# Optimization experiments

Measured on AMD Instinct MI355X. Metric: run time of the kernel, lower is better.

The kernel has to match this reference:

```python
import jax, jax.numpy as jnp
from jax import lax
import numpy as np

EPS = 1e-5
NH = 16  # attention heads (c // 16 with c = 256)


def _qconv(x, mod, phase, padding=0, groups=1):
    """Quaternion conv: real weight = modulus * cos(phase), applied per quaternion component.
    x: (B, C, Q, H, W) -> (B, O, Q, H, W)"""
    w = mod * jnp.cos(phase)
    B, C, Qd, H, W = x.shape
    xr = jnp.transpose(x, (0, 2, 1, 3, 4)).reshape(B * Qd, C, H, W)
    y = lax.conv_general_dilated(xr, w, (1, 1), [(padding, padding)] * 2,
                                 dimension_numbers=('NCHW', 'OIHW', 'NCHW'),
                                 feature_group_count=groups)
    O, Ho, Wo = y.shape[1], y.shape[2], y.shape[3]
    return jnp.transpose(y.reshape(B, Qd, O, Ho, Wo), (0, 2, 1, 3, 4))


def _bn(x):
    # IQBN/VQBN: per-channel normalization over (batch, quaternion, spatial), no affine
    m = x.mean(axis=(0, 2, 3, 4), keepdims=True)
    v = x.var(axis=(0, 2, 3, 4), keepdims=True)
    return (x - m) * lax.rsqrt(v + EPS)


def _attn(x, qkv_m, qkv_p, aproj_m, aproj_p, pe_m, pe_p):
    # QAttention: per-component multi-head self-attention over spatial tokens
    B, C, Qd, H, W = x.shape
    kd = C // NH
    qkv = _qconv(x, qkv_m, qkv_p)  # (B, 3C, Q, H, W)
    q, k, v = jnp.split(qkv, 3, axis=1)
    q = q.reshape(B, NH, kd, Qd, H * W)
    k = k.reshape(B, NH, kd, Qd, H * W)
    v = v.reshape(B, NH, kd, Qd, H * W)
    scores = jnp.einsum('bhcqn,bhcqm->bhqnm', q, k) * (kd ** -0.5)
    a = jax.nn.softmax(scores, axis=-1)
    out = jnp.einsum('bhqnm,bhdqm->bhdqn', a, v).reshape(B, C, Qd, H, W)
    # proj + depthwise positional conv on the input
    return _qconv(out, aproj_m, aproj_p) + _qconv(x, pe_m, pe_p, padding=1, groups=C)


def _psa(x, qkv_m, qkv_p, aproj_m, aproj_p, pe_m, pe_p, ffn1_m, ffn1_p, ffn2_m, ffn2_p):
    a = _attn(x, qkv_m, qkv_p, aproj_m, aproj_p, pe_m, pe_p) + x  # attn shortcut
    h = jax.nn.relu(_bn(_qconv(a, ffn1_m, ffn1_p)))
    f = _bn(_qconv(h, ffn2_m, ffn2_p))
    return f + a  # ffn shortcut


def _msab(x, guide, ec_m, ec_p, gl_w, gl_b, mproj_m, mproj_p):
    # MaxSigmoidAttnBlock (nh=1): global sigmoid gate per (batch, quaternion component)
    B, C, Qd, H, W = x.shape
    e = jax.nn.relu(_bn(_qconv(x, ec_m, ec_p)))  # (B, ec, Q, H, W)
    g = guide @ gl_w.T + gl_b                     # (B, ec)
    ec = g.shape[-1]
    a = jnp.einsum('bcqhw,bc->bq', e, g) / jnp.sqrt(jnp.asarray(ec * H * W, jnp.float32))
    a = jax.nn.sigmoid(a)  # scale param = 1.0 (scale=False)
    e = e * a[:, None, :, None, None]
    return jax.nn.relu(_bn(_qconv(e, mproj_m, mproj_p, padding=1)))


def _forward(x, guide, cv1_m, cv1_p, qkv_m, qkv_p, aproj_m, aproj_p, pe_m, pe_p,
             ffn1_m, ffn1_p, ffn2_m, ffn2_p, ec_m, ec_p, gl_w, gl_b,
             mproj_m, mproj_p, cv2_m, cv2_p):
    y = jax.nn.relu(_bn(_qconv(x, cv1_m, cv1_p)))       # (B, 2c, Q, H, W)
    a, b = jnp.split(y, 2, axis=1)                       # each (B, c, Q, H, W)
    p = _psa(b, qkv_m, qkv_p, aproj_m, aproj_p, pe_m, pe_p,
             ffn1_m, ffn1_p, ffn2_m, ffn2_p)
    m = _msab(p, guide, ec_m, ec_p, gl_w, gl_b, mproj_m, mproj_p)
    cat = jnp.concatenate([a, b, p, m], axis=1)          # (B, 4c, Q, H, W)
    return jax.nn.relu(_bn(_qconv(cat, cv2_m, cv2_p)))   # (B, c2, Q, H, W)


def setup_inputs():
    B, C1, Qd, H, W = 2, 512, 4, 24, 24
    c = 256; ecd = 128; gc = 512; C2 = 512
    ks = jax.random.split(jax.random.key(0), 24)
    def rp(k, shape, s=0.02):
        return s * jax.random.normal(k, shape, dtype=jnp.float32)
    return {
        'x': jax.random.normal(ks[0], (B, C1, Qd, H, W), dtype=jnp.float32),
        'guide': jax.random.normal(ks[1], (B, gc), dtype=jnp.float32),
        'cv1_m': rp(ks[2], (2 * c, C1, 1, 1)),
        'cv1_p': rp(ks[3], (2 * c, C1, 1, 1), 0.1),
        'qkv_m': rp(ks[4], (3 * c, c, 1, 1)),
        'qkv_p': rp(ks[5], (3 * c, c, 1, 1), 0.1),
        'aproj_m': rp(ks[6], (c, c, 1, 1)),
        'aproj_p': rp(ks[7], (c, c, 1, 1), 0.1),
        'pe_m': rp(ks[8], (c, 1, 3, 3)),
        'pe_p': rp(ks[9], (c, 1, 3, 3), 0.1),
        'ffn1_m': rp(ks[10], (2 * c, c, 1, 1)),
        'ffn1_p': rp(ks[11], (2 * c, c, 1, 1), 0.1),
        'ffn2_m': rp(ks[12], (c, 2 * c, 1, 1)),
        'ffn2_p': rp(ks[13], (c, 2 * c, 1, 1), 0.1),
        'ec_m': rp(ks[14], (ecd, c, 1, 1)),
        'ec_p': rp(ks[15], (ecd, c, 1, 1), 0.1),
        'gl_w': rp(ks[16], (ecd, gc), 0.05),
        'gl_b': jnp.zeros((ecd,), dtype=jnp.float32),
        'mproj_m': rp(ks[17], (c, ecd, 3, 3)),
        'mproj_p': rp(ks[18], (c, ecd, 3, 3), 0.1),
        'cv2_m': rp(ks[19], (C2, 4 * c, 1, 1)),
        'cv2_p': rp(ks[20], (C2, 4 * c, 1, 1), 0.1),
    }


def reference(x, guide, cv1_m, cv1_p, qkv_m, qkv_p, aproj_m, aproj_p, pe_m, pe_p,
              ffn1_m, ffn1_p, ffn2_m, ffn2_p, ec_m, ec_p, gl_w, gl_b,
              mproj_m, mproj_p, cv2_m, cv2_p):
    return _forward(x, guide, cv1_m, cv1_p, qkv_m, qkv_p, aproj_m, aproj_p, pe_m, pe_p,
                    ffn1_m, ffn1_p, ffn2_m, ffn2_p, ec_m, ec_p, gl_w, gl_b,
                    mproj_m, mproj_p, cv2_m, cv2_p)
```

## Files before the change

### kernel.cpp

```cpp
#include <hip/hip_runtime.h>
#include <math.h>

typedef __bf16 bf16x8 __attribute__((ext_vector_type(8)));
typedef float f32x4 __attribute__((ext_vector_type(4)));
typedef unsigned short u16;
typedef unsigned int u32;

__device__ __forceinline__ u16 f2bf(float f) {
  u32 u = __float_as_uint(f);
  u32 r = u + 0x7FFF + ((u >> 16) & 1);
  return (u16)(r >> 16);
}
__device__ __forceinline__ float bf2f(u16 h) { return __uint_as_float(((u32)h) << 16); }

static constexpr size_t OB_WBF = 0;
static constexpr size_t OB_WPE = 3276800;
static constexpr size_t OB_ST  = 3286016;
static constexpr size_t OB_GV  = 3310592;
static constexpr size_t OB_GACC= 3311616;
static constexpr size_t OB_CAT = 3311872;
static constexpr size_t OB_YA  = OB_CAT + 9437184;
static constexpr size_t OB_U1  = OB_YA + 9437184;
static constexpr size_t OB_U2  = OB_U1 + 4718592;
static constexpr size_t OB_U3  = OB_U2 + 14155776;
static constexpr size_t OB_AOB = OB_U3 + 4718592;
static constexpr size_t OB_A1B = OB_AOB + 2359296;
static constexpr size_t WS_TOTAL = OB_A1B + 2359296;

struct HeadP {
  const float* m[8]; const float* p[8]; u16* wout;
  const float* pem; const float* pep; float* peout;
  const float* x; u16* xb;
  const float* guide; const float* glw; const float* glb; float* gv;
  int cum[9]; int nwp;
};
__global__ __launch_bounds__(256) void k_head(HeadP P) {
  int bid = blockIdx.x;
  if (bid < P.nwp) {
    int i = bid * 256 + threadIdx.x;
    if (i < 2304) {
      int tap = i >> 8, c = i & 255;
      P.peout[i] = P.pem[c * 9 + tap] * cosf(P.pep[c * 9 + tap]);
    }
    if (i >= P.cum[8]) return;
    int s = 0;
    while (s < 7 && i >= P.cum[s + 1]) s++;
    int j = i - P.cum[s];
    int src = j;
    if (s == 6) {
      int o = j / 1152, r = j % 1152, kk = r >> 7, cc = r & 127;
      src = (o * 128 + cc) * 9 + kk;
    }
    P.wout[i] = f2bf(P.m[s][src] * cosf(P.p[s][src]));
    return;
  }
  bid -= P.nwp;
  if (bid < 2304) {
    int mt = bid % 18; bid /= 18;
    int ct = bid % 16; bid /= 16;
    int q = bid & 3, b = bid >> 2;
    __shared__ float tile[32][33];
    int tj = threadIdx.x & 31, ti = threadIdx.x >> 5;
    const float* xp = P.x + (((size_t)(b * 512 + ct * 32) * 4 + q) * 576) + mt * 32;
#pragma unroll
    for (int ii = 0; ii < 4; ii++)
      tile[ti + ii * 8][tj] = xp[(size_t)(ti + ii * 8) * 4 * 576 + tj];
    __syncthreads();
    u16* yp = P.xb + ((size_t)b * 2304 + q * 576 + mt * 32) * 512 + ct * 32;
#pragma unroll
    for (int mm = 0; mm < 4; mm++)
      yp[(size_t)(mm * 8 + ti) * 512 + tj] = f2bf(tile[tj][mm * 8 + ti]);
    return;
  }
  bid -= 2304;
  int wv = threadIdx.x >> 6, lane = threadIdx.x & 63;
  int be = bid * 4 + wv;
  int b = be >> 7, e = be & 127;
  const float* gr = P.guide + b * 512;
  const float* wr = P.glw + e * 512;
  float s = 0.f;
  for (int c = lane; c < 512; c += 64) s = fmaf(gr[c], wr[c], s);
#pragma unroll
  for (int off = 32; off > 0; off >>= 1) s += __shfl_down(s, off, 64);
  if (lane == 0) P.gv[be] = s + P.glb[e];
}

struct GemmP {
  const u16* W; const u16* X; u16* Yb; float* St;
  const u16* CAT; const float* W9;
  const u16* EF; const float* GA;
  long long xOff[8];
  int lda, O, K, M, G;
};

template <int BM, int NWO, int WO, int WM, int MODE>
__global__ __launch_bounds__(256) void k_gemm(GemmP P) {
  constexpr int FO = WO / 16, FM = WM / 16;
  constexpr int OBLK = NWO * WO;
  constexpr int ABYTES = OBLK * 128, BBYTES = BM * 128;
  __shared__ __align__(16) char lds[2 * ABYTES + 2 * BBYTES];
  const int mt = P.M / BM;
  const int ot = P.O / OBLK;
  int bid = blockIdx.x;
  const int g = bid / (mt * ot);
  const int rr = bid % (mt * ot);
  const int ob = (rr / mt) * OBLK;
  const int mb = (rr % mt) * BM;
  const int t = threadIdx.x, lane = t & 63, wave = t >> 6;
  const int wo = (wave % NWO) * WO, wm = (wave / NWO) * WM;
  const u16* Wp = P.W + (size_t)ob * P.K;
  const u16* Xp = (MODE == 2) ? nullptr : (P.X + P.xOff[g] + (size_t)mb * P.lda);

  float gt = 0.f;
  int bq2304 = 0;
  if constexpr (MODE == 2) {
    bq2304 = (g >> 2) * 2304 + (g & 3) * 576;
    float a = P.GA[g] / sqrtf(73728.0f);
    gt = 1.f / (1.f + __expf(-a));
  }

  f32x4 acc[FO][FM] = {};
  float vreg[2][8];

  auto stageA = [&](int tb, int k0) {
#pragma unroll
    for (int i = 0; i < OBLK * 8 / 256; i++) {
      int s = (i * 4 + wave) * 64 + lane;
      int row = s >> 3;
      int kg = (s & 7) ^ (row & 7);
      const u16* src = Wp + (size_t)row * P.K + k0 + kg * 8;
      __builtin_amdgcn_global_load_lds(
          (const __attribute__((address_space(1))) u32*)src,
          (__attribute__((address_space(3))) u32*)(lds + tb * ABYTES + (size_t)(i * 4 + wave) * 1024),
          16, 0, 0);
    }
  };
  auto stageB = [&](int tb, int k0) {
#pragma unroll
    for (int i = 0; i < BM * 8 / 256; i++) {
      int s = (i * 4 + wave) * 64 + lane;
      int row = s >> 3;
      int kg = (s & 7) ^ (row & 7);
      const u16* src = Xp + (size_t)row * P.lda + k0 + kg * 8;
      __builtin_amdgcn_global_load_lds(
          (const __attribute__((address_space(1))) u32*)src,
          (__attribute__((address_space(3))) u32*)(lds + 2 * ABYTES + tb * BBYTES +
                                                   (size_t)(i * 4 + wave) * 1024),
          16, 0, 0);
    }
  };
  auto loadEF = [&](int k0) {
#pragma unroll
    for (int i = 0; i < 2; i++) {
      int s = t + i * 256;
      int row = s >> 3, kg = s & 7;
      int k = k0 + kg * 8;
      int kk = k >> 7, cc = k & 127;
      int n = mb + row;
      int h = n / 24 + kk / 3 - 1, w = n % 24 + kk % 3 - 1;
      if (h >= 0 && h < 24 && w >= 0 && w < 24) {
        const u16* ep = P.EF + ((size_t)(bq2304 + h * 24 + w)) * 128 + cc;
        ushort4 v0 = *(const ushort4*)ep;
        ushort4 v1 = *(const ushort4*)(ep + 4);
        vreg[i][0] = bf2f(v0.x); vreg[i][1] = bf2f(v0.y);
        vreg[i][2] = bf2f(v0.z); vreg[i][3] = bf2f(v0.w);
        vreg[i][4] = bf2f(v1.x); vreg[i][5] = bf2f(v1.y);
        vreg[i][6] = bf2f(v1.z); vreg[i][7] = bf2f(v1.w);
      } else {
#pragma unroll
        for (int j = 0; j < 8; j++) vreg[i][j] = 0.f;
      }
    }
  };
  auto writeB = [&](int tb) {
#pragma unroll
    for (int i = 0; i < 2; i++) {
      int s = t + i * 256;
      int row = s >> 3, kg = s & 7;
      u16 pk[8];
#pragma unroll
      for (int j = 0; j < 8; j++) pk[j] = f2bf(vreg[i][j] * gt);
      *(uint4*)&lds[2 * ABYTES + tb * BBYTES + (((row << 3) + (kg ^ (row & 7))) << 4)] =
          *(uint4*)pk;
    }
  };

  const int nt = P.K >> 6;
  stageA(0, 0);
  if constexpr (MODE != 2) {
    stageB(0, 0);
  } else {
    loadEF(0);
    writeB(0);
  }
  __syncthreads();

  for (int tt = 0; tt < nt; tt++) {
    const int cur = tt & 1, nxt = cur ^ 1;
    const bool more = (tt + 1) < nt;
    if (more) {
      stageA(nxt, (tt + 1) << 6);
      if constexpr (MODE != 2) stageB(nxt, (tt + 1) << 6);
      else loadEF((tt + 1) << 6);
    }
    const char* bA = lds + cur * ABYTES;
    const char* bB = lds + 2 * ABYTES + cur * BBYTES;
#pragma unroll
    for (int kk = 0; kk < 2; kk++) {
      int kgl = kk * 4 + (lane >> 4);
      bf16x8 af[FO], bfm[FM];
#pragma unroll
      for (int fo = 0; fo < FO; fo++) {
        int row = wo + fo * 16 + (lane & 15);
        af[fo] = *(bf16x8*)&bA[((row << 3) + (kgl ^ (row & 7))) << 4];
      }
#pragma unroll
      for (int fm = 0; fm < FM; fm++) {
        int row = wm + fm * 16 + (lane & 15);
        bfm[fm] = *(bf16x8*)&bB[((row << 3) + (kgl ^ (row & 7))) << 4];
      }
#pragma unroll
      for (int fo = 0; fo < FO; fo++)
#pragma unroll
        for (int fm = 0; fm < FM; fm++)
          acc[fo][fm] = __builtin_amdgcn_mfma_f32_16x16x32_bf16(af[fo], bfm[fm], acc[fo][fm], 0, 0, 0);
    }
    if (more) {
      if constexpr (MODE == 2) writeB(nxt);
      __syncthreads();
    }
  }

  size_t ybase = (size_t)g * P.M * P.O;
#pragma unroll
  for (int fo = 0; fo < FO; fo++) {
    int ow = ob + wo + fo * 16 + ((lane >> 4) << 2);
#pragma unroll
    for (int fm = 0; fm < FM; fm++) {
      int m = mb + wm + fm * 16 + (lane & 15);
      f32x4 v = acc[fo][fm];
      if constexpr (MODE == 1) {
        size_t tokc = ((size_t)g * 2304 + m) * 1024 + 256 + ow;
        ushort4 cv = *(const ushort4*)&P.CAT[tokc];
        v[0] += bf2f(cv.x); v[1] += bf2f(cv.y); v[2] += bf2f(cv.z); v[3] += bf2f(cv.w);
        int q_ = m / 576, hw_ = m % 576, h_ = hw_ / 24, w_ = hw_ % 24;
        size_t rowb = ((size_t)g * 2304 + q_ * 576) * 1024 + 256 + ow;
#pragma unroll
        for (int tp = 0; tp < 9; tp++) {
          int hh = h_ + tp / 3 - 1, ww = w_ + tp % 3 - 1;
          if (hh < 0 || hh > 23 || ww < 0 || ww > 23) continue;
          ushort4 tv = *(const ushort4*)&P.CAT[rowb + (size_t)(hh * 24 + ww) * 1024];
          f32x4 wt = *(const f32x4*)&P.W9[tp * 256 + ow];
          v[0] = fmaf(wt[0], bf2f(tv.x), v[0]);
          v[1] = fmaf(wt[1], bf2f(tv.y), v[1]);
          v[2] = fmaf(wt[2], bf2f(tv.z), v[2]);
          v[3] = fmaf(wt[3], bf2f(tv.w), v[3]);
        }
        acc[fo][fm] = v;
      }
      size_t off = ybase + (size_t)m * P.O + ow;
      ushort4 r;
      r.x = f2bf(v[0]); r.y = f2bf(v[1]); r.z = f2bf(v[2]); r.w = f2bf(v[3]);
      *(ushort4*)&P.Yb[off] = r;
    }
  }

  if (P.St) {
#pragma unroll
    for (int fo = 0; fo < FO; fo++) {
      float sv[4], qv[4];
#pragma unroll
      for (int j = 0; j < 4; j++) { sv[j] = 0.f; qv[j] = 0.f; }
#pragma unroll
      for (int fm = 0; fm < FM; fm++)
#pragma unroll
        for (int j = 0; j < 4; j++) {
          float a = acc[fo][fm][j];
          sv[j] += a;
          qv[j] = fmaf(a, a, qv[j]);
        }
#pragma unroll
      for (int j = 0; j < 4; j++) {
#pragma unroll
        for (int mk = 1; mk < 16; mk <<= 1) {
          sv[j] += __shfl_xor(sv[j], mk, 64);
          qv[j] += __shfl_xor(qv[j], mk, 64);
        }
      }
      if ((lane & 15) == 0) {
        int o = ob + wo + fo * 16 + ((lane >> 4) << 2);
#pragma unroll
        for (int j = 0; j < 4; j++) {
          atomicAdd(&P.St[2 * (o + j)], sv[j]);
          atomicAdd(&P.St[2 * (o + j) + 1], qv[j]);
        }
      }
    }
  }
}

struct NormP {
  const u16* X; const float* st; const u16* AddB;
  u16* Yb; u16* Yfb; const float* gv; float* gacc;
  long long ybOff[8];
  int ldyb, O, G, M, relu;
  float n;
};
__global__ __launch_bounds__(256) void k_norm(NormP P) {
  int O4 = P.O >> 2;
  long long idx = (long long)blockIdx.x * 256 + threadIdx.x;
  if (idx >= (long long)P.G * P.M * O4) return;
  int c4 = (int)(idx % O4);
  long long gm = idx / O4;
  int m = (int)(gm % P.M);
  int g = (int)(gm / P.M);
  size_t off = (size_t)gm * P.O + c4 * 4;
  ushort4 xv = *(const ushort4*)&P.X[off];
  f32x4 v = {bf2f(xv.x), bf2f(xv.y), bf2f(xv.z), bf2f(xv.w)};
  float inv_n = 1.0f / P.n;
#pragma unroll
  for (int j = 0; j < 4; j++) {
    int c = c4 * 4 + j;
    float mean = P.st[2 * c] * inv_n;
    float var = P.st[2 * c + 1] * inv_n - mean * mean;
    v[j] = (v[j] - mean) * rsqrtf(var + 1e-5f);
  }
  if (P.AddB) {
    ushort4 av = *(const ushort4*)(P.AddB + off);
    v[0] += bf2f(av.x); v[1] += bf2f(av.y); v[2] += bf2f(av.z); v[3] += bf2f(av.w);
  }
  if (P.relu) {
#pragma unroll
    for (int j = 0; j < 4; j++) v[j] = fmaxf(v[j], 0.f);
  }
  ushort4 r;
  r.x = f2bf(v[0]); r.y = f2bf(v[1]); r.z = f2bf(v[2]); r.w = f2bf(v[3]);
  if (P.Yb) *(ushort4*)(P.Yb + P.ybOff[g] + (size_t)m * P.ldyb + c4 * 4) = r;
  if (P.Yfb) *(ushort4*)(P.Yfb + off) = r;
  if (P.gacc) {
    float gs = 0.f;
#pragma unroll
    for (int j = 0; j < 4; j++) gs = fmaf(v[j], P.gv[g * 128 + c4 * 4 + j], gs);
#pragma unroll
    for (int mk = 1; mk < 64; mk <<= 1) gs += __shfl_xor(gs, mk, 64);
    __shared__ float t1[4];
    int lane = threadIdx.x & 63, wv = threadIdx.x >> 6;
    if (lane == 0) t1[wv] = gs;
    __syncthreads();
    if (threadIdx.x == 0)
      atomicAdd(&P.gacc[g * 4 + m / 576], t1[0] + t1[1] + t1[2] + t1[3]);
  }
}

__global__ __launch_bounds__(256) void k_normT(const u16* X, const float* st, float* out) {
  int bid = blockIdx.x;
  int ot = bid & 15;
  int mt = (bid >> 4) % 72;
  int b = bid / 1152;
  int mb = mt * 32, ob = ot * 32;
  __shared__ float tile[32][33];
  int c = threadIdx.x & 31, r = threadIdx.x >> 5;
#pragma unroll
  for (int i = 0; i < 4; i++) {
    int row = r + i * 8;
    tile[row][c] = bf2f(X[((size_t)b * 2304 + mb + row) * 512 + ob + c]);
  }
  __syncthreads();
  float inv_n = 1.0f / 4608.0f;
#pragma unroll
  for (int i = 0; i < 4; i++) {
    int o = ob + r + i * 8;
    float mean = st[2 * o] * inv_n;
    float var = st[2 * o + 1] * inv_n - mean * mean;
    float rs = rsqrtf(var + 1e-5f);
    float v = fmaxf((tile[c][r + i * 8] - mean) * rs, 0.f);
    out[((size_t)(b * 512 + o)) * 2304 + mb + c] = v;
  }
}

__global__ __launch_bounds__(256) void k_attn(const u16* qkv, u16* ao) {
  int bid = blockIdx.x;
  int tq = bid % 3; int u = bid / 3;
  int qd = u & 3; u >>= 2;
  int head = u & 15, b = u >> 4;
  int t = threadIdx.x, lane = t & 63, wv = t >> 6;
  int g = lane >> 4, q = lane & 15;
  size_t tok0 = (size_t)b * 2304 + qd * 576;
  const u16* QKV = qkv + tok0 * 768;

  __shared__ __align__(16) char shm[50176];
  u16* Kl = (u16*)(shm);
  u16* VT = (u16*)(shm + 27648);
  u16* Pl = (u16*)(shm + 46080 + wv * 1024);

  for (int i = t; i < 1152; i += 256) {
    int m = i >> 1, half = i & 1;
    const u16* src = QKV + (size_t)m * 768 + 256 + head * 16 + half * 8;
    u16 tmp[8];
    *(uint4*)tmp = *(const uint4*)src;
    ushort4 lo, hi;
    lo.x = f2bf(bf2f(tmp[0]) * 0.25f); lo.y = f2bf(bf2f(tmp[1]) * 0.25f);
    lo.z = f2bf(bf2f(tmp[2]) * 0.25f); lo.w = f2bf(bf2f(tmp[3]) * 0.25f);
    hi.x = f2bf(bf2f(tmp[4]) * 0.25f); hi.y = f2bf(bf2f(tmp[5]) * 0.25f);
    hi.z = f2bf(bf2f(tmp[6]) * 0.25f); hi.w = f2bf(bf2f(tmp[7]) * 0.25f);
    u16* dst = Kl + m * 24 + half * 8;
    *(ushort4*)dst = lo;
    *(ushort4*)(dst + 4) = hi;
  }
  for (int mm = t; mm < 576; mm += 256) {
    const u16* src = QKV + (size_t)mm * 768 + 512 + head * 16;
    u16 tmp[16];
    *(uint4*)tmp = *(const uint4*)src;
    *(uint4*)(tmp + 8) = *(const uint4*)(src + 8);
    u16* dst = VT + (mm >> 3) * 128 + (mm & 7);
#pragma unroll
    for (int d = 0; d < 16; d++) dst[d * 8] = tmp[d];
  }
  __syncthreads();

#pragma unroll 1
  for (int i = 0; i < 3; i++) {
    int tl = wv * 3 + i;
    int qbase = tq * 192 + tl * 16;
    bf16x8 qf = {};
    if (g < 2)
      qf = *(const bf16x8*)(QKV + (size_t)(qbase + q) * 768 + head * 16 + g * 8);

    f32x4 acc_o = {};
    float ssum = 0.f;

    for (int ch = 0; ch < 18; ch++) {
      int m0 = ch * 32;
      f32x4 s[2];
#pragma unroll
      for (int h = 0; h < 2; h++) {
        bf16x8 kf = {};
        if (g < 2)
          kf = *(const bf16x8*)(Kl + (size_t)(m0 + h * 16 + q) * 24 + g * 8);
        f32x4 z = {};
        s[h] = __builtin_amdgcn_mfma_f32_16x16x32_bf16(kf, qf, z, 0, 0, 0);
      }
#pragma unroll
      for (int h = 0; h < 2; h++) {
        float p0 = __expf(s[h][0]);
        float p1 = __expf(s[h][1]);
        float p2 = __expf(s[h][2]);
        float p3 = __expf(s[h][3]);
        ssum += (p0 + p1) + (p2 + p3);
        ushort4 w;
        w.x = f2bf(p0); w.y = f2bf(p1); w.z = f2bf(p2); w.w = f2bf(p3);
        *(ushort4*)(Pl + ((h * 2 + (g >> 1)) * 16 + q) * 8 + (g & 1) * 4) = w;
      }
      bf16x8 va = *(const bf16x8*)(VT + ((m0 >> 3) + g) * 128 + q * 8);
      bf16x8 pa = *(const bf16x8*)(Pl + (g * 16 + q) * 8);
      acc_o = __builtin_amdgcn_mfma_f32_16x16x32_bf16(va, pa, acc_o, 0, 0, 0);
    }

    ssum += __shfl_xor(ssum, 16, 64);
    ssum += __shfl_xor(ssum, 32, 64);
    float inv = 1.f / ssum;
    u16* op = ao + (tok0 + qbase + q) * 256 + head * 16 + g * 4;
    ushort4 r;
    r.x = f2bf(acc_o[0] * inv);
    r.y = f2bf(acc_o[1] * inv);
    r.z = f2bf(acc_o[2] * inv);
    r.w = f2bf(acc_o[3] * inv);
    *(ushort4*)op = r;
  }
}

extern "C" void kernel_launch(void* const* d_in, const int* in_sizes, int n_in,
                              void* d_out, int out_size, void* d_ws, size_t ws_size,
                              hipStream_t stream) {
  if (ws_size < WS_TOTAL) return;
  char* ws = (char*)d_ws;
  u16* WB = (u16*)(ws + OB_WBF);
  float* WPE = (float*)(ws + OB_WPE);
  float* STB = (float*)(ws + OB_ST);
  float* GV = (float*)(ws + OB_GV);
  float* GACC = (float*)(ws + OB_GACC);
  u16* CATB = (u16*)(ws + OB_CAT);
  u16* YAB = (u16*)(ws + OB_YA);
  u16* XBF = (u16*)(ws + OB_U1);
  u16* QKVB = (u16*)(ws + OB_U2);
  u16* EFB = (u16*)(ws + OB_U2 + 10616832);
  u16* HB = (u16*)(ws + OB_U3);
  u16* AOB = (u16*)(ws + OB_AOB);
  u16* A1B = (u16*)(ws + OB_A1B);
  float* out = (float*)d_out;

  hipMemsetAsync(ws + OB_ST, 0, OB_CAT - OB_ST, stream);

  {
    HeadP p;
    const int mi[8] = {2, 4, 6, 10, 12, 14, 18, 20};
    const int sz[8] = {262144, 196608, 65536, 131072, 131072, 32768, 294912, 524288};
    int c = 0;
    for (int i = 0; i < 8; i++) {
      p.m[i] = (const float*)d_in[mi[i]];
      p.p[i] = (const float*)d_in[mi[i] + 1];
      p.cum[i] = c;
      c += sz[i];
    }
    p.cum[8] = c;
    p.wout = WB;
    p.pem = (const float*)d_in[8];
    p.pep = (const float*)d_in[9];
    p.peout = WPE;
    p.x = (const float*)d_in[0];
    p.xb = XBF;
    p.guide = (const float*)d_in[1];
    p.glw = (const float*)d_in[16];
    p.glb = (const float*)d_in[17];
    p.gv = GV;
    p.nwp = (c + 255) / 256;
    int grid = p.nwp + 2304 + 64;
    k_head<<<grid, 256, 0, stream>>>(p);
  }

  auto gemm = [&](int mode, size_t wOff, int O, int K, int M, int G,
                  const u16* X, long long xs, long long xadd, int lda,
                  u16* Yb, int si) {
    GemmP p;
    p.W = WB + wOff; p.X = X; p.Yb = Yb;
    p.St = (si >= 0) ? (STB + si * 1024) : nullptr;
    p.CAT = CATB; p.W9 = WPE; p.EF = EFB; p.GA = GACC;
    p.lda = lda; p.O = O; p.K = K; p.M = M; p.G = G;
    for (int g = 0; g < 8; g++) p.xOff[g] = (long long)(g < G ? g : 0) * xs + xadd;
    int grid = G * (O / 128) * (M / 64);
    if (mode == 0)
      k_gemm<64, 4, 32, 64, 0><<<grid, 256, 0, stream>>>(p);
    else if (mode == 1)
      k_gemm<64, 4, 32, 64, 1><<<grid, 256, 0, stream>>>(p);
    else
      k_gemm<64, 4, 32, 64, 2><<<grid, 256, 0, stream>>>(p);
  };
  auto norm = [&](const u16* X, int si, int O, int G, int M, const u16* AddB,
                  u16* Yb, int ldyb, const long long* ybOff, u16* Yfb, int relu,
                  const float* gv, float* gacc) {
    NormP p;
    p.X = X; p.st = STB + si * 1024; p.AddB = AddB; p.Yb = Yb; p.Yfb = Yfb;
    p.gv = gv; p.gacc = gacc;
    p.ldyb = ldyb; p.O = O; p.G = G; p.M = M; p.relu = relu;
    p.n = (float)(G * M);
    for (int g = 0; g < 8; g++) p.ybOff[g] = ybOff ? ybOff[(g < G) ? g : 0] : 0;
    long long total = (long long)G * M * (O / 4);
    k_norm<<<(int)((total + 255) / 256), 256, 0, stream>>>(p);
  };

  gemm(0, 0, 512, 512, 2304, 2, XBF, 2304LL * 512, 0, 512, YAB, 0);
  { long long yo[2] = {0, 2304LL * 1024};
    norm(YAB, 0, 512, 2, 2304, nullptr, CATB, 1024, yo, nullptr, 1, nullptr, nullptr); }

  gemm(0, 262144, 768, 256, 2304, 2, CATB, 2304LL * 1024, 256, 1024, QKVB, -1);
  k_attn<<<384, 256, 0, stream>>>(QKVB, AOB);
  gemm(1, 458752, 256, 256, 2304, 2, AOB, 2304LL * 256, 0, 256, A1B, -1);

  gemm(0, 524288, 512, 256, 2304, 2, A1B, 2304LL * 256, 0, 256, YAB, 1);
  { long long yo[2] = {0, 2304LL * 512};
    norm(YAB, 1, 512, 2, 2304, nullptr, HB, 512, yo, nullptr, 1, nullptr, nullptr); }

  gemm(0, 655360, 256, 512, 2304, 2, HB, 2304LL * 512, 0, 512, YAB, 2);
  { long long yo[2] = {512, 2304LL * 1024 + 512};
    norm(YAB, 2, 256, 2, 2304, A1B, CATB, 1024, yo, nullptr, 0, nullptr, nullptr); }

  gemm(0, 786432, 128, 256, 2304, 2, CATB, 2304LL * 1024, 512, 1024, YAB, 3);
  norm(YAB, 3, 128, 2, 2304, nullptr, nullptr, 0, nullptr, EFB, 1, GV, GACC);

  gemm(2, 819200, 256, 1152, 576, 8, nullptr, 0, 0, 0, YAB, 4);
  { long long yo[8];
    for (int g = 0; g < 8; g++)
      yo[g] = (long long)(g >> 2) * 2304 * 1024 + (long long)(g & 3) * 576 * 1024 + 768;
    norm(YAB, 4, 256, 8, 576, nullptr, CATB, 1024, yo, nullptr, 1, nullptr, nullptr); }

  gemm(0, 1114112, 512, 1024, 2304, 2, CATB, 2304LL * 1024, 0, 1024, YAB, 5);
  k_normT<<<2304, 256, 0, stream>>>(YAB, STB + 5 * 1024, out);
}
```

Before: 259.3 us.

## Fuse batch-norm epilogues into GEMMs using an atomic grid-wide barrier

```diff
diff --git a/kernel.cpp b/kernel.cpp
--- a/kernel.cpp
+++ b/kernel.cpp
@@ -18,6 +18,7 @@
 static constexpr size_t OB_ST  = 3286016;
 static constexpr size_t OB_GV  = 3310592;
 static constexpr size_t OB_GACC= 3311616;
+static constexpr size_t OB_CTR = 3311744;
 static constexpr size_t OB_CAT = 3311872;
 static constexpr size_t OB_YA  = OB_CAT + 9437184;
 static constexpr size_t OB_U1  = OB_YA + 9437184;
@@ -89,11 +90,12 @@
   const u16* W; const u16* X; u16* Yb; float* St;
   const u16* CAT; const float* W9;
   const u16* EF; const float* GA;
-  long long xOff[8];
-  int lda, O, K, M, G;
+  const u16* AddB; const float* gv; float* gacc; float* outF; u32* ctr;
+  long long xOff[8]; long long yOff2[8];
+  int lda, O, K, M, G, ldyb, relu, nblk;
 };
 
-template <int BM, int NWO, int WO, int WM, int MODE>
+template <int BM, int NWO, int WO, int WM, int MODE, int NEPI>
 __global__ __launch_bounds__(256) void k_gemm(GemmP P) {
   constexpr int FO = WO / 16, FM = WM / 16;
   constexpr int OBLK = NWO * WO;
@@ -231,41 +233,42 @@
     }
   }
 
+  const int lane15 = lane & 15, laneh = (lane >> 4) << 2;
   size_t ybase = (size_t)g * P.M * P.O;
-#pragma unroll
-  for (int fo = 0; fo < FO; fo++) {
-    int ow = ob + wo + fo * 16 + ((lane >> 4) << 2);
-#pragma unroll
-    for (int fm = 0; fm < FM; fm++) {
-      int m = mb + wm + fm * 16 + (lane & 15);
-      f32x4 v = acc[fo][fm];
-      if constexpr (MODE == 1) {
-        size_t tokc = ((size_t)g * 2304 + m) * 1024 + 256 + ow;
-        ushort4 cv = *(const ushort4*)&P.CAT[tokc];
-        v[0] += bf2f(cv.x); v[1] += bf2f(cv.y); v[2] += bf2f(cv.z); v[3] += bf2f(cv.w);
-        int q_ = m / 576, hw_ = m % 576, h_ = hw_ / 24, w_ = hw_ % 24;
-        size_t rowb = ((size_t)g * 2304 + q_ * 576) * 1024 + 256 + ow;
-#pragma unroll
-        for (int tp = 0; tp < 9; tp++) {
-          int hh = h_ + tp / 3 - 1, ww = w_ + tp % 3 - 1;
-          if (hh < 0 || hh > 23 || ww < 0 || ww > 23) continue;
-          ushort4 tv = *(const ushort4*)&P.CAT[rowb + (size_t)(hh * 24 + ww) * 1024];
-          f32x4 wt = *(const f32x4*)&P.W9[tp * 256 + ow];
-          v[0] = fmaf(wt[0], bf2f(tv.x), v[0]);
-          v[1] = fmaf(wt[1], bf2f(tv.y), v[1]);
-          v[2] = fmaf(wt[2], bf2f(tv.z), v[2]);
-          v[3] = fmaf(wt[3], bf2f(tv.w), v[3]);
+
+  if constexpr (NEPI == 0) {
+#pragma unroll
+    for (int fo = 0; fo < FO; fo++) {
+      int ow = ob + wo + fo * 16 + laneh;
+#pragma unroll
+      for (int fm = 0; fm < FM; fm++) {
+        int m = mb + wm + fm * 16 + lane15;
+        f32x4 v = acc[fo][fm];
+        if constexpr (MODE == 1) {
+          size_t tokc = ((size_t)g * 2304 + m) * 1024 + 256 + ow;
+          ushort4 cv = *(const ushort4*)&P.CAT[tokc];
+          v[0] += bf2f(cv.x); v[1] += bf2f(cv.y); v[2] += bf2f(cv.z); v[3] += bf2f(cv.w);
+          int q_ = m / 576, hw_ = m % 576, h_ = hw_ / 24, w_ = hw_ % 24;
+          size_t rowb = ((size_t)g * 2304 + q_ * 576) * 1024 + 256 + ow;
+#pragma unroll
+          for (int tp = 0; tp < 9; tp++) {
+            int hh = h_ + tp / 3 - 1, ww = w_ + tp % 3 - 1;
+            if (hh < 0 || hh > 23 || ww < 0 || ww > 23) continue;
+            ushort4 tv = *(const ushort4*)&P.CAT[rowb + (size_t)(hh * 24 + ww) * 1024];
+            f32x4 wt = *(const f32x4*)&P.W9[tp * 256 + ow];
+            v[0] = fmaf(wt[0], bf2f(tv.x), v[0]);
+            v[1] = fmaf(wt[1], bf2f(tv.y), v[1]);
+            v[2] = fmaf(wt[2], bf2f(tv.z), v[2]);
+            v[3] = fmaf(wt[3], bf2f(tv.w), v[3]);
+          }
         }
-        acc[fo][fm] = v;
-      }
-      size_t off = ybase + (size_t)m * P.O + ow;
-      ushort4 r;
-      r.x = f2bf(v[0]); r.y = f2bf(v[1]); r.z = f2bf(v[2]); r.w = f2bf(v[3]);
-      *(ushort4*)&P.Yb[off] = r;
-    }
-  }
-
-  if (P.St) {
+        size_t off = ybase + (size_t)m * P.O + ow;
+        ushort4 r;
+        r.x = f2bf(v[0]); r.y = f2bf(v[1]); r.z = f2bf(v[2]); r.w = f2bf(v[3]);
+        *(ushort4*)&P.Yb[off] = r;
+      }
+    }
+  } else {
 #pragma unroll
     for (int fo = 0; fo < FO; fo++) {
       float sv[4], qv[4];
@@ -287,8 +290,8 @@
           qv[j] += __shfl_xor(qv[j], mk, 64);
         }
       }
-      if ((lane & 15) == 0) {
-        int o = ob + wo + fo * 16 + ((lane >> 4) << 2);
+      if (lane15 == 0) {
+        int o = ob + wo + fo * 16 + laneh;
 #pragma unroll
         for (int j = 0; j < 4; j++) {
           atomicAdd(&P.St[2 * (o + j)], sv[j]);
@@ -296,85 +299,77 @@
         }
       }
     }
-  }
-}
-
-struct NormP {
-  const u16* X; const float* st; const u16* AddB;
-  u16* Yb; u16* Yfb; const float* gv; float* gacc;
-  long long ybOff[8];
-  int ldyb, O, G, M, relu;
-  float n;
-};
-__global__ __launch_bounds__(256) void k_norm(NormP P) {
-  int O4 = P.O >> 2;
-  long long idx = (long long)blockIdx.x * 256 + threadIdx.x;
-  if (idx >= (long long)P.G * P.M * O4) return;
-  int c4 = (int)(idx % O4);
-  long long gm = idx / O4;
-  int m = (int)(gm % P.M);
-  int g = (int)(gm / P.M);
-  size_t off = (size_t)gm * P.O + c4 * 4;
-  ushort4 xv = *(const ushort4*)&P.X[off];
-  f32x4 v = {bf2f(xv.x), bf2f(xv.y), bf2f(xv.z), bf2f(xv.w)};
-  float inv_n = 1.0f / P.n;
-#pragma unroll
-  for (int j = 0; j < 4; j++) {
-    int c = c4 * 4 + j;
-    float mean = P.st[2 * c] * inv_n;
-    float var = P.st[2 * c + 1] * inv_n - mean * mean;
-    v[j] = (v[j] - mean) * rsqrtf(var + 1e-5f);
-  }
-  if (P.AddB) {
-    ushort4 av = *(const ushort4*)(P.AddB + off);
-    v[0] += bf2f(av.x); v[1] += bf2f(av.y); v[2] += bf2f(av.z); v[3] += bf2f(av.w);
-  }
-  if (P.relu) {
-#pragma unroll
-    for (int j = 0; j < 4; j++) v[j] = fmaxf(v[j], 0.f);
-  }
-  ushort4 r;
-  r.x = f2bf(v[0]); r.y = f2bf(v[1]); r.z = f2bf(v[2]); r.w = f2bf(v[3]);
-  if (P.Yb) *(ushort4*)(P.Yb + P.ybOff[g] + (size_t)m * P.ldyb + c4 * 4) = r;
-  if (P.Yfb) *(ushort4*)(P.Yfb + off) = r;
-  if (P.gacc) {
+    __threadfence();
+    __syncthreads();
+    if (t == 0) {
+      atomicAdd(P.ctr, 1u);
+      while (atomicAdd(P.ctr, 0u) < (u32)P.nblk) __builtin_amdgcn_s_sleep(32);
+    }
+    __syncthreads();
+    __threadfence();
+
+    const float inv_n = 1.0f / 4608.0f;
+    float mn[FO][4], rs[FO][4];
+#pragma unroll
+    for (int fo = 0; fo < FO; fo++) {
+      int o = ob + wo + fo * 16 + laneh;
+#pragma unroll
+      for (int j = 0; j < 4; j++) {
+        float mean = P.St[2 * (o + j)] * inv_n;
+        float var = P.St[2 * (o + j) + 1] * inv_n - mean * mean;
+        mn[fo][j] = mean;
+        rs[fo][j] = rsqrtf(var + 1e-5f);
+      }
+    }
     float gs = 0.f;
 #pragma unroll
-    for (int j = 0; j < 4; j++) gs = fmaf(v[j], P.gv[g * 128 + c4 * 4 + j], gs);
-#pragma unroll
-    for (int mk = 1; mk < 64; mk <<= 1) gs += __shfl_xor(gs, mk, 64);
-    __shared__ float t1[4];
-    int lane = threadIdx.x & 63, wv = threadIdx.x >> 6;
-    if (lane == 0) t1[wv] = gs;
-    __syncthreads();
-    if (threadIdx.x == 0)
-      atomicAdd(&P.gacc[g * 4 + m / 576], t1[0] + t1[1] + t1[2] + t1[3]);
-  }
-}
-
-__global__ __launch_bounds__(256) void k_normT(const u16* X, const float* st, float* out) {
-  int bid = blockIdx.x;
-  int ot = bid & 15;
-  int mt = (bid >> 4) % 72;
-  int b = bid / 1152;
-  int mb = mt * 32, ob = ot * 32;
-  __shared__ float tile[32][33];
-  int c = threadIdx.x & 31, r = threadIdx.x >> 5;
-#pragma unroll
-  for (int i = 0; i < 4; i++) {
-    int row = r + i * 8;
-    tile[row][c] = bf2f(X[((size_t)b * 2304 + mb + row) * 512 + ob + c]);
-  }
-  __syncthreads();
-  float inv_n = 1.0f / 4608.0f;
-#pragma unroll
-  for (int i = 0; i < 4; i++) {
-    int o = ob + r + i * 8;
-    float mean = st[2 * o] * inv_n;
-    float var = st[2 * o + 1] * inv_n - mean * mean;
-    float rs = rsqrtf(var + 1e-5f);
-    float v = fmaxf((tile[c][r + i * 8] - mean) * rs, 0.f);
-    out[((size_t)(b * 512 + o)) * 2304 + mb + c] = v;
+    for (int fo = 0; fo < FO; fo++) {
+      int ow = ob + wo + fo * 16 + laneh;
+#pragma unroll
+      for (int fm = 0; fm < FM; fm++) {
+        int m = mb + wm + fm * 16 + lane15;
+        f32x4 v = acc[fo][fm];
+#pragma unroll
+        for (int j = 0; j < 4; j++) v[j] = (v[j] - mn[fo][j]) * rs[fo][j];
+        if constexpr (NEPI == 1) {
+          if (P.AddB) {
+            ushort4 av = *(const ushort4*)(P.AddB + ybase + (size_t)m * P.O + ow);
+            v[0] += bf2f(av.x); v[1] += bf2f(av.y); v[2] += bf2f(av.z); v[3] += bf2f(av.w);
+          }
+          if (P.relu) {
+#pragma unroll
+            for (int j = 0; j < 4; j++) v[j] = fmaxf(v[j], 0.f);
+          }
+          ushort4 r;
+          r.x = f2bf(v[0]); r.y = f2bf(v[1]); r.z = f2bf(v[2]); r.w = f2bf(v[3]);
+          *(ushort4*)(P.Yb + P.yOff2[g] + (size_t)m * P.ldyb + ow) = r;
+        } else if constexpr (NEPI == 2) {
+#pragma unroll
+          for (int j = 0; j < 4; j++) v[j] = fmaxf(v[j], 0.f);
+          ushort4 r;
+          r.x = f2bf(v[0]); r.y = f2bf(v[1]); r.z = f2bf(v[2]); r.w = f2bf(v[3]);
+          *(ushort4*)(P.Yb + ybase + (size_t)m * 128 + ow) = r;
+#pragma unroll
+          for (int j = 0; j < 4; j++) gs = fmaf(v[j], P.gv[g * 128 + ow + j], gs);
+        } else {
+#pragma unroll
+          for (int j = 0; j < 4; j++) {
+            float x = fmaxf(v[j], 0.f);
+            P.outF[(size_t)(g * 512 + ow + j) * 2304 + m] = x;
+          }
+        }
+      }
+    }
+    if constexpr (NEPI == 2) {
+#pragma unroll
+      for (int mk = 1; mk < 64; mk <<= 1) gs += __shfl_xor(gs, mk, 64);
+      float* red = (float*)lds;
+      __syncthreads();
+      if (lane == 0) red[wave] = gs;
+      __syncthreads();
+      if (t == 0)
+        atomicAdd(&P.gacc[g * 4 + mb / 576], red[0] + red[1] + red[2] + red[3]);
+    }
   }
 }
 
@@ -479,8 +474,8 @@
   float* STB = (float*)(ws + OB_ST);
   float* GV = (float*)(ws + OB_GV);
   float* GACC = (float*)(ws + OB_GACC);
+  u32* CTR = (u32*)(ws + OB_CTR);
   u16* CATB = (u16*)(ws + OB_CAT);
-  u16* YAB = (u16*)(ws + OB_YA);
   u16* XBF = (u16*)(ws + OB_U1);
   u16* QKVB = (u16*)(ws + OB_U2);
   u16* EFB = (u16*)(ws + OB_U2 + 10616832);
@@ -518,61 +513,57 @@
     k_head<<<grid, 256, 0, stream>>>(p);
   }
 
-  auto gemm = [&](int mode, size_t wOff, int O, int K, int M, int G,
+  auto gemm = [&](int mode, int nepi, size_t wOff, int O, int K, int M, int G,
                   const u16* X, long long xs, long long xadd, int lda,
-                  u16* Yb, int si) {
+                  u16* Yb, int si, const long long* yo2, int ldyb, int relu,
+                  const u16* AddB) {
     GemmP p;
     p.W = WB + wOff; p.X = X; p.Yb = Yb;
     p.St = (si >= 0) ? (STB + si * 1024) : nullptr;
+    p.ctr = (si >= 0) ? (CTR + si) : nullptr;
     p.CAT = CATB; p.W9 = WPE; p.EF = EFB; p.GA = GACC;
+    p.AddB = AddB; p.gv = GV; p.gacc = GACC; p.outF = out;
     p.lda = lda; p.O = O; p.K = K; p.M = M; p.G = G;
-    for (int g = 0; g < 8; g++) p.xOff[g] = (long long)(g < G ? g : 0) * xs + xadd;
+    p.ldyb = ldyb; p.relu = relu;
+    for (int g = 0; g < 8; g++) {
+      p.xOff[g] = (long long)(g < G ? g : 0) * xs + xadd;
+      p.yOff2[g] = yo2 ? yo2[(g < G) ? g : 0] : 0;
+    }
     int grid = G * (O / 128) * (M / 64);
-    if (mode == 0)
-      k_gemm<64, 4, 32, 64, 0><<<grid, 256, 0, stream>>>(p);
-    else if (mode == 1)
-      k_gemm<64, 4, 32, 64, 1><<<grid, 256, 0, stream>>>(p);
+    p.nblk = grid;
+    if (mode == 0 && nepi == 0)
+      k_gemm<64, 4, 32, 64, 0, 0><<<grid, 256, 0, stream>>>(p);
+    else if (mode == 1 && nepi == 0)
+      k_gemm<64, 4, 32, 64, 1, 0><<<grid, 256, 0, stream>>>(p);
+    else if (mode == 0 && nepi == 1)
+      k_gemm<64, 4, 32, 64, 0, 1><<<grid, 256, 0, stream>>>(p);
+    else if (mode == 2 && nepi == 1)
+      k_gemm<64, 4, 32, 64, 2, 1><<<grid, 256, 0, stream>>>(p);
+    else if (mode == 0 && nepi == 2)
+      k_gemm<64, 4, 32, 64, 0, 2><<<grid, 256, 0, stream>>>(p);
     else
-      k_gemm<64, 4, 32, 64, 2><<<grid, 256, 0, stream>>>(p);
+      k_gemm<64, 4, 32, 64, 0, 3><<<grid, 256, 0, stream>>>(p);
   };
-  auto norm = [&](const u16* X, int si, int O, int G, int M, const u16* AddB,
-                  u16* Yb, int ldyb, const long long* ybOff, u16* Yfb, int relu,
-                  const float* gv, float* gacc) {
-    NormP p;
-    p.X = X; p.st = STB + si * 1024; p.AddB = AddB; p.Yb = Yb; p.Yfb = Yfb;
-    p.gv = gv; p.gacc = gacc;
-    p.ldyb = ldyb; p.O = O; p.G = G; p.M = M; p.relu = relu;
-    p.n = (float)(G * M);
-    for (int g = 0; g < 8; g++) p.ybOff[g] = ybOff ? ybOff[(g < G) ? g : 0] : 0;
-    long long total = (long long)G * M * (O / 4);
-    k_norm<<<(int)((total + 255) / 256), 256, 0, stream>>>(p);
-  };
-
-  gemm(0, 0, 512, 512, 2304, 2, XBF, 2304LL * 512, 0, 512, YAB, 0);
+
   { long long yo[2] = {0, 2304LL * 1024};
-    norm(YAB, 0, 512, 2, 2304, nullptr, CATB, 1024, yo, nullptr, 1, nullptr, nullptr); }
-
-  gemm(0, 262144, 768, 256, 2304, 2, CATB, 2304LL * 1024, 256, 1024, QKVB, -1);
+    gemm(0, 1, 0, 512, 512, 2304, 2, XBF, 2304LL * 512, 0, 512, CATB, 0, yo, 1024, 1, nullptr); }
+
+  gemm(0, 0, 262144, 768, 256, 2304, 2, CATB, 2304LL * 1024, 256, 1024, QKVB, -1, nullptr, 0, 0, nullptr);
   k_attn<<<384, 256, 0, stream>>>(QKVB, AOB);
-  gemm(1, 458752, 256, 256, 2304, 2, AOB, 2304LL * 256, 0, 256, A1B, -1);
-
-  gemm(0, 524288, 512, 256, 2304, 2, A1B, 2304LL * 256, 0, 256, YAB, 1);
+  gemm(1, 0, 458752, 256, 256, 2304, 2, AOB, 2304LL * 256, 0, 256, A1B, -1, nullptr, 0, 0, nullptr);
+
   { long long yo[2] = {0, 2304LL * 512};
-    norm(YAB, 1, 512, 2, 2304, nullptr, HB, 512, yo, nullptr, 1, nullptr, nullptr); }
-
-  gemm(0, 655360, 256, 512, 2304, 2, HB, 2304LL * 512, 0, 512, YAB, 2);
+    gemm(0, 1, 524288, 512, 256, 2304, 2, A1B, 2304LL * 256, 0, 256, HB, 1, yo, 512, 1, nullptr); }
+
   { long long yo[2] = {512, 2304LL * 1024 + 512};
-    norm(YAB, 2, 256, 2, 2304, A1B, CATB, 1024, yo, nullptr, 0, nullptr, nullptr); }
-
-  gemm(0, 786432, 128, 256, 2304, 2, CATB, 2304LL * 1024, 512, 1024, YAB, 3);
-  norm(YAB, 3, 128, 2, 2304, nullptr, nullptr, 0, nullptr, EFB, 1, GV, GACC);
-
-  gemm(2, 819200, 256, 1152, 576, 8, nullptr, 0, 0, 0, YAB, 4);
+    gemm(0, 1, 655360, 256, 512, 2304, 2, HB, 2304LL * 512, 0, 512, CATB, 2, yo, 1024, 0, A1B); }
+
+  gemm(0, 2, 786432, 128, 256, 2304, 2, CATB, 2304LL * 1024, 512, 1024, EFB, 3, nullptr, 0, 1, nullptr);
+
   { long long yo[8];
     for (int g = 0; g < 8; g++)
       yo[g] = (long long)(g >> 2) * 2304 * 1024 + (long long)(g & 3) * 576 * 1024 + 768;
-    norm(YAB, 4, 256, 8, 576, nullptr, CATB, 1024, yo, nullptr, 1, nullptr, nullptr); }
-
-  gemm(0, 1114112, 512, 1024, 2304, 2, CATB, 2304LL * 1024, 0, 1024, YAB, 5);
-  k_normT<<<2304, 256, 0, stream>>>(YAB, STB + 5 * 1024, out);
+    gemm(2, 1, 819200, 256, 1152, 576, 8, nullptr, 0, 0, 0, CATB, 4, yo, 1024, 1, nullptr); }
+
+  gemm(0, 3, 1114112, 512, 1024, 2304, 2, CATB, 2304LL * 1024, 0, 1024, nullptr, 5, nullptr, 0, 1, nullptr);
 }
```

After: 408.5 us. +57.5%, slower.
